# Kernel optimization log

Measured on AMD Instinct MI355X. Metric: run time of the kernel, lower is better.

The kernel has to match this reference:

```python
import jax, jax.numpy as jnp
import numpy as np

TAU = 0.02
M = 5  # len(modality_types) + 1; modality 0 == padding


def setup_inputs() -> dict:
    B, Q, S, D = 64, 32, 256, 128
    key = jax.random.key(0)
    k0, k1, k2, k3, k4 = jax.random.split(key, 5)
    q = jax.random.normal(k0, (B, Q, D), dtype=jnp.float32)
    q = q / jnp.linalg.norm(q, axis=-1, keepdims=True)
    d = jax.random.normal(k1, (B, S, D), dtype=jnp.float32)
    d = d / jnp.linalg.norm(d, axis=-1, keepdims=True)
    # guarantee every modality 0..M-1 appears in each doc (first M tokens)
    head = jnp.tile(jnp.arange(M, dtype=jnp.int32), (B, 1))
    rest = jax.random.randint(k2, (B, S - M), 0, M, dtype=jnp.int32)
    modality_ids = jnp.concatenate([head, rest], axis=1)
    query_types = jax.random.randint(k3, (B,), 1, M, dtype=jnp.int32)  # in [1, M-1]
    lengths = jax.random.randint(k4, (B,), Q // 2, Q + 1)
    query_mask = jnp.arange(Q)[None, :] < lengths[:, None]
    return {"query_emb": q, "doc_emb": d, "modality_ids": modality_ids,
            "query_types": query_types, "query_mask": query_mask}


def _loss(query_emb, doc_emb, modality_ids, query_types, query_mask):
    B = query_emb.shape[0]
    idx = jnp.arange(B)
    # token-level similarity: (B, C, Q, S)
    base = jnp.einsum('bqd,csd->bcqs', query_emb, doc_emb)
    qnorm = jnp.maximum(query_mask.sum(axis=1), 1).astype(base.dtype)  # (B,)

    # agg (ColBERT max-sim): max over non-pad doc tokens, masked query sum
    nonpad = (modality_ids != 0)[None, :, None, :]
    agg_max = jnp.where(nonpad, base, -jnp.inf).max(axis=-1)           # (B, C, Q)
    sim = (agg_max * query_mask[:, None, :].astype(base.dtype)).sum(axis=-1)
    sim = sim / qnorm[:, None]                                          # (B, C)

    # _all_modality_sims: segmented max over s per modality, then sum over q
    per_mod = []
    for m in range(M):
        mask_m = (modality_ids == m)[None, :, None, :]
        per_mod.append(jnp.where(mask_m, base, -jnp.inf).max(axis=-1).sum(axis=-1))
    sims = jnp.stack(per_mod, axis=-1)                                  # (B, C, M)
    sims = sims / qnorm[:, None, None]

    # replace diagonal with the query's own modality score
    sim_fixed = sim.at[idx, idx].set(sims[idx, idx, query_types])

    # hard negatives: all (doc, modality) pairs except pad modality and own positive
    all_modal = sims.reshape(B, B * M)
    keep_mask = jnp.ones((B, B * M), dtype=bool)
    keep_mask = keep_mask.at[:, 0::M].set(False)
    keep_mask = keep_mask.at[idx, idx * M + query_types].set(False)
    n_keep = B * M - B - 1  # exact per-row count (query_types >= 1, no overlap)
    order = jnp.argsort((~keep_mask).astype(jnp.int32), axis=1, stable=True)[:, :n_keep]
    extras = jnp.take_along_axis(all_modal, order, axis=1)              # (B, n_keep)

    logits = jnp.concatenate([sim_fixed, extras], axis=1) / TAU
    # cross entropy with labels = arange(B) (positive is column b)
    return (jax.nn.logsumexp(logits, axis=1) - logits[idx, idx]).mean()


def reference(query_emb, doc_emb, modality_ids, query_types, query_mask):
    return _loss(query_emb, doc_emb, modality_ids, query_types, query_mask)
```

## Files before the change

kernel.cpp:

```cpp
#include <hip/hip_runtime.h>
#include <math.h>

#define TAU_F 0.02f
#define NB 64
#define NQ 32
#define NS 256
#define ND 128
#define MAXT 12
#define PERMSTRIDE 384

typedef __bf16 bf16x8 __attribute__((ext_vector_type(8)));
typedef float f32x16 __attribute__((ext_vector_type(16)));

#define OFF_TILEMOD 0u
#define OFF_TCOUNT  4096u
#define OFF_DFRAG   16384u
#define OFF_QFRAG   6307840u
#define OFF_SIMOUT  6832128u
#define OFF_RED     6914048u

__global__ __launch_bounds__(256) void
prep_frag_kernel(const float* __restrict__ qemb, const float* __restrict__ demb,
                 const int* __restrict__ mod,
                 __bf16* __restrict__ qfrag, __bf16* __restrict__ dfrag,
                 int* __restrict__ tilemod_g, int* __restrict__ tcount_g,
                 int* __restrict__ red) {
    int blk = blockIdx.x;
    int tid = threadIdx.x;
    int lane = tid & 63, wv = tid >> 6;
    int li32 = lane & 31, kh = lane >> 5;

    if (blk == 0 && tid == 0) { red[0] = 0; ((float*)red)[16] = 0.f; }

    if (blk >= NB) {
        int b = blk - NB;
#pragma unroll
        for (int i = 0; i < 2; ++i) {
            int kc = wv * 2 + i;
            int k0 = kc * 16 + kh * 8;
            const float* src = qemb + ((size_t)b * NQ + li32) * ND + k0;
            float4 a = *(const float4*)src;
            float4 bq = *(const float4*)(src + 4);
            bf16x8 o;
            o[0] = (__bf16)a.x;  o[1] = (__bf16)a.y;  o[2] = (__bf16)a.z;  o[3] = (__bf16)a.w;
            o[4] = (__bf16)bq.x; o[5] = (__bf16)bq.y; o[6] = (__bf16)bq.z; o[7] = (__bf16)bq.w;
            *(bf16x8*)(qfrag + (((size_t)b * 8 + kc) * 64 + lane) * 8) = o;
        }
        return;
    }

    int c = blk;
    __shared__ int smod[NS];
    __shared__ int sperm[PERMSTRIDE];
    __shared__ int counts[5], firsts[5], offs[5], padded[5];
    __shared__ int stilemod[MAXT];
    __shared__ int sT;

    if (tid < 5) { counts[tid] = 0; firsts[tid] = NS; }
    __syncthreads();
    int m_tok = mod[c * NS + tid];
    smod[tid] = m_tok;
    if (m_tok) { atomicAdd(&counts[m_tok], 1); atomicMin(&firsts[m_tok], tid); }
    __syncthreads();
    if (tid == 0) {
        int pos = 0;
        for (int m = 1; m <= 4; ++m) {
            offs[m] = pos;
            int p = (counts[m] + 31) & ~31;
            padded[m] = p;
            for (int t = pos >> 5; t < (pos + p) >> 5; ++t) stilemod[t] = m;
            pos += p;
        }
        sT = pos >> 5;
        tcount_g[c] = pos >> 5;
    }
    __syncthreads();
    if (m_tok) {
        int rank = 0;
        for (int s = 0; s < tid; ++s) rank += (smod[s] == m_tok);
        sperm[offs[m_tok] + rank] = tid;
    }
    if (tid < 4) {
        int m = tid + 1;
        for (int p = counts[m]; p < padded[m]; ++p) sperm[offs[m] + p] = firsts[m];
    }
    __syncthreads();
    int T = sT;
    if (tid < T) tilemod_g[c * MAXT + tid] = stilemod[tid];

    for (int kc = wv; kc < 8; kc += 4) {
        int k0 = kc * 16 + kh * 8;
        for (int t = 0; t < T; ++t) {
            int srow = sperm[t * 32 + li32];
            const float* src = demb + ((size_t)c * NS + srow) * ND + k0;
            float4 a = *(const float4*)src;
            float4 bq = *(const float4*)(src + 4);
            bf16x8 o;
            o[0] = (__bf16)a.x;  o[1] = (__bf16)a.y;  o[2] = (__bf16)a.z;  o[3] = (__bf16)a.w;
            o[4] = (__bf16)bq.x; o[5] = (__bf16)bq.y; o[6] = (__bf16)bq.z; o[7] = (__bf16)bq.w;
            *(bf16x8*)(dfrag + (((size_t)(c * MAXT + t) * 8 + kc) * 64 + lane) * 8) = o;
        }
    }
}

__global__ __launch_bounds__(256) void
main_kernel(const __bf16* __restrict__ dfrag, const __bf16* __restrict__ qfrag,
            const int* __restrict__ tilemod, const int* __restrict__ tcount,
            const int* __restrict__ qmask, float* __restrict__ simout) {
    int blk = blockIdx.x;
    int c  = (blk & 7) * 8 + (blk >> 8);
    int bp = (blk >> 3) & 31;
    int b0 = bp * 2;
    int tid = threadIdx.x;
    int lane = tid & 63, wv = tid >> 6;

    bf16x8 bfrag[2][8];
#pragma unroll
    for (int bi = 0; bi < 2; ++bi)
#pragma unroll
        for (int kc = 0; kc < 8; ++kc)
            bfrag[bi][kc] = *(const bf16x8*)(qfrag + (((size_t)(b0 + bi) * 8 + kc) * 64 + lane) * 8);

    float vmax[2][4];
#pragma unroll
    for (int bi = 0; bi < 2; ++bi)
#pragma unroll
        for (int m = 0; m < 4; ++m) vmax[bi][m] = -1e30f;

    int T = tcount[c];
    for (int t = wv; t < T; t += 4) {
        bf16x8 af[8];
#pragma unroll
        for (int kc = 0; kc < 8; ++kc)
            af[kc] = *(const bf16x8*)(dfrag + (((size_t)(c * MAXT + t) * 8 + kc) * 64 + lane) * 8);
        int tm = tilemod[c * MAXT + t];
#pragma unroll
        for (int bi = 0; bi < 2; ++bi) {
            f32x16 acc = {0.f,0.f,0.f,0.f,0.f,0.f,0.f,0.f,0.f,0.f,0.f,0.f,0.f,0.f,0.f,0.f};
#pragma unroll
            for (int kc = 0; kc < 8; ++kc)
                acc = __builtin_amdgcn_mfma_f32_32x32x16_bf16(af[kc], bfrag[bi][kc], acc, 0, 0, 0);
            float v = acc[0];
#pragma unroll
            for (int r = 1; r < 16; ++r) v = fmaxf(v, acc[r]);
            v = fmaxf(v, __shfl_xor(v, 32, 64));
            switch (tm) {
            case 1:  vmax[bi][0] = fmaxf(vmax[bi][0], v); break;
            case 2:  vmax[bi][1] = fmaxf(vmax[bi][1], v); break;
            case 3:  vmax[bi][2] = fmaxf(vmax[bi][2], v); break;
            default: vmax[bi][3] = fmaxf(vmax[bi][3], v); break;
            }
        }
    }

    __shared__ float lv[4][2][4][32];
    if (lane < 32) {
#pragma unroll
        for (int bi = 0; bi < 2; ++bi)
#pragma unroll
            for (int m = 0; m < 4; ++m) lv[wv][bi][m][lane] = vmax[bi][m];
    }
    __syncthreads();
    __shared__ float l2s[2][4][32];
    {
        int bi = tid >> 7, m = (tid >> 5) & 3, q = tid & 31;
        float v = fmaxf(fmaxf(lv[0][bi][m][q], lv[1][bi][m][q]),
                        fmaxf(lv[2][bi][m][q], lv[3][bi][m][q]));
        l2s[bi][m][q] = v;
    }
    __syncthreads();
    if (tid < 64) {
        int bi = tid >> 5, q = tid & 31;
        float m1 = l2s[bi][0][q], m2 = l2s[bi][1][q];
        float m3 = l2s[bi][2][q], m4 = l2s[bi][3][q];
        int b = b0 + bi;
        float agg = fmaxf(fmaxf(m1, m2), fmaxf(m3, m4));
        float s0 = (qmask[b * NQ + q] != 0) ? agg : 0.f;
        float s1 = m1, s2 = m2, s3 = m3, s4 = m4;
#pragma unroll
        for (int off = 16; off >= 1; off >>= 1) {
            s0 += __shfl_xor(s0, off, 64);
            s1 += __shfl_xor(s1, off, 64);
            s2 += __shfl_xor(s2, off, 64);
            s3 += __shfl_xor(s3, off, 64);
            s4 += __shfl_xor(s4, off, 64);
        }
        if (q == 0) {
            float* o = simout + ((size_t)b * NB + c) * 5;
            o[0] = s0; o[1] = s1; o[2] = s2; o[3] = s3; o[4] = s4;
        }
    }
}

__global__ __launch_bounds__(256) void
loss_kernel(const float* __restrict__ simout, const int* __restrict__ qtypes,
            const int* __restrict__ qmask, int* __restrict__ red,
            float* __restrict__ out) {
    int r = blockIdx.x;
    int tid = threadIdx.x;
    int lane = tid & 63, wv = tid >> 6;

    __shared__ float sv[320];
    for (int i = tid; i < 320; i += 256) sv[i] = simout[(size_t)r * 320 + i];

    __shared__ int scnt;
    if (wv == 0) {
        int on = (lane < NQ) ? (qmask[r * NQ + lane] != 0) : 0;
        unsigned long long bal = __ballot(on);
        if (lane == 0) scnt = __popcll(bal);
    }
    __syncthreads();
    int cq = scnt;
    float scale = 1.0f / (TAU_F * (float)(cq > 0 ? cq : 1));
    int skip = r * 5;

    __shared__ float wred[4];
    float mx = -1e30f;
    for (int i = tid; i < 320; i += 256)
        if (i != skip) mx = fmaxf(mx, sv[i] * scale);
#pragma unroll
    for (int off = 32; off >= 1; off >>= 1) mx = fmaxf(mx, __shfl_xor(mx, off, 64));
    if (lane == 0) wred[wv] = mx;
    __syncthreads();
    mx = fmaxf(fmaxf(wred[0], wred[1]), fmaxf(wred[2], wred[3]));

    float sum = 0.f;
    for (int i = tid; i < 320; i += 256)
        if (i != skip) sum += expf(sv[i] * scale - mx);
#pragma unroll
    for (int off = 32; off >= 1; off >>= 1) sum += __shfl_xor(sum, off, 64);
    __syncthreads();
    if (lane == 0) wred[wv] = sum;
    __syncthreads();

    if (tid == 0) {
        float tot = wred[0] + wred[1] + wred[2] + wred[3];
        float pos = sv[r * 5 + qtypes[r]] * scale;
        float lr = (logf(tot) + mx - pos) * (1.0f / NB);
        float* acc = (float*)red + 16;
        float ret = atomicAdd(acc, lr);
        int bump = 1 + (ret > 1e37f ? 1 : 0);
        int old = atomicAdd(red, bump);
        if (old == NB - 1) {
            float v = atomicAdd(acc, 0.f);
            out[0] = v;
        }
    }
}

extern "C" void kernel_launch(void* const* d_in, const int* in_sizes, int n_in,
                              void* d_out, int out_size, void* d_ws, size_t ws_size,
                              hipStream_t stream) {
    const float* qemb   = (const float*)d_in[0];
    const float* demb   = (const float*)d_in[1];
    const int*   mod    = (const int*)d_in[2];
    const int*   qtypes = (const int*)d_in[3];
    const int*   qmask  = (const int*)d_in[4];

    char* ws = (char*)d_ws;
    int*    tilemod = (int*)(ws + OFF_TILEMOD);
    int*    tcount  = (int*)(ws + OFF_TCOUNT);
    __bf16* dfrag   = (__bf16*)(ws + OFF_DFRAG);
    __bf16* qfrag   = (__bf16*)(ws + OFF_QFRAG);
    float*  simout  = (float*)(ws + OFF_SIMOUT);
    int*    red     = (int*)(ws + OFF_RED);

    prep_frag_kernel<<<2 * NB, 256, 0, stream>>>(qemb, demb, mod, qfrag, dfrag,
                                                 tilemod, tcount, red);
    main_kernel<<<2048, 256, 0, stream>>>(dfrag, qfrag, tilemod, tcount, qmask, simout);
    loss_kernel<<<NB, 256, 0, stream>>>(simout, qtypes, qmask, red, (float*)d_out);
}
```

Measured before the change: 94.91 us.

## Fuse loss computation into main kernel via last-block-done counters per query pair

Removes the separate loss kernel launch. Each main-kernel block bumps a per-query-pair counter, and the last of the 64 blocks for that pair reads the pair's similarity rows with atomic loads and computes both cross-entropy terms. A global counter then picks the final block, which writes the mean. This saves one launch and its dependency gap, at the cost of extra atomics and a serialized tail in the last blocks, plus a reliance on memory ordering between blocks.

Result: slower. 101.1 us (+6.5%).

```diff
diff --git a/kernel.cpp b/kernel.cpp
--- a/kernel.cpp
+++ b/kernel.cpp
@@ -30,7 +30,11 @@
     int lane = tid & 63, wv = tid >> 6;
     int li32 = lane & 31, kh = lane >> 5;
 
-    if (blk == 0 && tid == 0) { red[0] = 0; ((float*)red)[16] = 0.f; }
+    if (blk == 0 && tid < 34) {
+        if (tid < 32) red[tid] = 0;
+        else if (tid == 32) red[32] = 0;
+        else ((float*)red)[48] = 0.f;
+    }
 
     if (blk >= NB) {
         int b = blk - NB;
@@ -106,7 +110,9 @@
 __global__ __launch_bounds__(256) void
 main_kernel(const __bf16* __restrict__ dfrag, const __bf16* __restrict__ qfrag,
             const int* __restrict__ tilemod, const int* __restrict__ tcount,
-            const int* __restrict__ qmask, float* __restrict__ simout) {
+            const int* __restrict__ qmask, const int* __restrict__ qtypes,
+            float* __restrict__ simout, int* __restrict__ red,
+            float* __restrict__ out) {
     int blk = blockIdx.x;
     int c  = (blk & 7) * 8 + (blk >> 8);
     int bp = (blk >> 3) & 31;
@@ -187,62 +193,70 @@
         }
         if (q == 0) {
             float* o = simout + ((size_t)b * NB + c) * 5;
-            o[0] = s0; o[1] = s1; o[2] = s2; o[3] = s3; o[4] = s4;
-        }
-    }
-}
-
-__global__ __launch_bounds__(256) void
-loss_kernel(const float* __restrict__ simout, const int* __restrict__ qtypes,
-            const int* __restrict__ qmask, int* __restrict__ red,
-            float* __restrict__ out) {
-    int r = blockIdx.x;
-    int tid = threadIdx.x;
-    int lane = tid & 63, wv = tid >> 6;
+            __hip_atomic_store(&o[0], s0, __ATOMIC_RELAXED, __HIP_MEMORY_SCOPE_AGENT);
+            __hip_atomic_store(&o[1], s1, __ATOMIC_RELAXED, __HIP_MEMORY_SCOPE_AGENT);
+            __hip_atomic_store(&o[2], s2, __ATOMIC_RELAXED, __HIP_MEMORY_SCOPE_AGENT);
+            __hip_atomic_store(&o[3], s3, __ATOMIC_RELAXED, __HIP_MEMORY_SCOPE_AGENT);
+            __hip_atomic_store(&o[4], s4, __ATOMIC_RELAXED, __HIP_MEMORY_SCOPE_AGENT);
+        }
+    }
+
+    __shared__ int swin;
+    __syncthreads();
+    if (tid == 0) swin = (atomicAdd(&red[bp], 1) == 63);
+    __syncthreads();
+    if (!swin) return;
 
     __shared__ float sv[320];
-    for (int i = tid; i < 320; i += 256) sv[i] = simout[(size_t)r * 320 + i];
-
+    __shared__ float wred[4];
     __shared__ int scnt;
-    if (wv == 0) {
-        int on = (lane < NQ) ? (qmask[r * NQ + lane] != 0) : 0;
-        unsigned long long bal = __ballot(on);
-        if (lane == 0) scnt = __popcll(bal);
-    }
-    __syncthreads();
-    int cq = scnt;
-    float scale = 1.0f / (TAU_F * (float)(cq > 0 ? cq : 1));
-    int skip = r * 5;
-
-    __shared__ float wred[4];
-    float mx = -1e30f;
-    for (int i = tid; i < 320; i += 256)
-        if (i != skip) mx = fmaxf(mx, sv[i] * scale);
-#pragma unroll
-    for (int off = 32; off >= 1; off >>= 1) mx = fmaxf(mx, __shfl_xor(mx, off, 64));
-    if (lane == 0) wred[wv] = mx;
-    __syncthreads();
-    mx = fmaxf(fmaxf(wred[0], wred[1]), fmaxf(wred[2], wred[3]));
-
-    float sum = 0.f;
-    for (int i = tid; i < 320; i += 256)
-        if (i != skip) sum += expf(sv[i] * scale - mx);
-#pragma unroll
-    for (int off = 32; off >= 1; off >>= 1) sum += __shfl_xor(sum, off, 64);
-    __syncthreads();
-    if (lane == 0) wred[wv] = sum;
-    __syncthreads();
-
+    float lr_sum = 0.f;
+#pragma unroll
+    for (int bi = 0; bi < 2; ++bi) {
+        int r = b0 + bi;
+        for (int i = tid; i < 320; i += 256)
+            sv[i] = __hip_atomic_load(&simout[(size_t)r * 320 + i],
+                                      __ATOMIC_RELAXED, __HIP_MEMORY_SCOPE_AGENT);
+        if (wv == 0) {
+            int on = (lane < NQ) ? (qmask[r * NQ + lane] != 0) : 0;
+            unsigned long long bal = __ballot(on);
+            if (lane == 0) scnt = __popcll(bal);
+        }
+        __syncthreads();
+        int cq = scnt;
+        float scale = 1.0f / (TAU_F * (float)(cq > 0 ? cq : 1));
+        int skip = r * 5;
+        float mx = -1e30f;
+        for (int i = tid; i < 320; i += 256)
+            if (i != skip) mx = fmaxf(mx, sv[i] * scale);
+#pragma unroll
+        for (int off = 32; off >= 1; off >>= 1) mx = fmaxf(mx, __shfl_xor(mx, off, 64));
+        if (lane == 0) wred[wv] = mx;
+        __syncthreads();
+        mx = fmaxf(fmaxf(wred[0], wred[1]), fmaxf(wred[2], wred[3]));
+        float sum = 0.f;
+        for (int i = tid; i < 320; i += 256)
+            if (i != skip) sum += expf(sv[i] * scale - mx);
+#pragma unroll
+        for (int off = 32; off >= 1; off >>= 1) sum += __shfl_xor(sum, off, 64);
+        __syncthreads();
+        if (lane == 0) wred[wv] = sum;
+        __syncthreads();
+        if (tid == 0) {
+            float tot = wred[0] + wred[1] + wred[2] + wred[3];
+            float pos = sv[r * 5 + qtypes[r]] * scale;
+            lr_sum += (logf(tot) + mx - pos) * (1.0f / NB);
+        }
+        __syncthreads();
+    }
     if (tid == 0) {
-        float tot = wred[0] + wred[1] + wred[2] + wred[3];
-        float pos = sv[r * 5 + qtypes[r]] * scale;
-        float lr = (logf(tot) + mx - pos) * (1.0f / NB);
-        float* acc = (float*)red + 16;
-        float ret = atomicAdd(acc, lr);
+        float* gacc = (float*)red + 48;
+        float ret = atomicAdd(gacc, lr_sum);
+        asm volatile("s_waitcnt vmcnt(0)" ::: "memory");
         int bump = 1 + (ret > 1e37f ? 1 : 0);
-        int old = atomicAdd(red, bump);
-        if (old == NB - 1) {
-            float v = atomicAdd(acc, 0.f);
+        int old = atomicAdd(&red[32], bump);
+        if (old == 31) {
+            float v = atomicAdd(gacc, 0.f);
             out[0] = v;
         }
     }
@@ -267,6 +281,6 @@
 
     prep_frag_kernel<<<2 * NB, 256, 0, stream>>>(qemb, demb, mod, qfrag, dfrag,
                                                  tilemod, tcount, red);
-    main_kernel<<<2048, 256, 0, stream>>>(dfrag, qfrag, tilemod, tcount, qmask, simout);
-    loss_kernel<<<NB, 256, 0, stream>>>(simout, qtypes, qmask, red, (float*)d_out);
+    main_kernel<<<2048, 256, 0, stream>>>(dfrag, qfrag, tilemod, tcount, qmask,
+                                          qtypes, simout, red, (float*)d_out);
 }
```

## Share doc tiles across waves via double-buffered LDS, split queries per wave

Applied to the files above, without the earlier changes.

Each block of the main kernel now handles one document and eight queries, with each wave owning two queries. The block streams the doc's 32-token tiles through a double-buffered shared-memory buffer, prefetching the next tile into registers while the current one is multiplied. This replaces per-wave global loads of a disjoint subset of tiles and the cross-wave shared-memory max reduction. The grid shrinks from 2048 to 512 blocks, so there is less parallelism, and each tile step now has a block-wide barrier, in exchange for four times the reuse of each doc tile.

New measurement: 90.65 us. -4.5%, faster.

```diff
diff --git a/kernel.cpp b/kernel.cpp
--- a/kernel.cpp
+++ b/kernel.cpp
@@ -103,16 +103,18 @@
     }
 }
 
-__global__ __launch_bounds__(256) void
+__global__ __launch_bounds__(256, 2) void
 main_kernel(const __bf16* __restrict__ dfrag, const __bf16* __restrict__ qfrag,
             const int* __restrict__ tilemod, const int* __restrict__ tcount,
             const int* __restrict__ qmask, float* __restrict__ simout) {
     int blk = blockIdx.x;
-    int c  = (blk & 7) * 8 + (blk >> 8);
-    int bp = (blk >> 3) & 31;
-    int b0 = bp * 2;
+    int xcd = blk & 7;
+    int idx = blk >> 3;
+    int c   = xcd * 8 + (idx & 7);
+    int bq  = idx >> 3;
     int tid = threadIdx.x;
     int lane = tid & 63, wv = tid >> 6;
+    int b0 = bq * 8 + wv * 2;
 
     bf16x8 bfrag[2][8];
 #pragma unroll
@@ -121,59 +123,68 @@
         for (int kc = 0; kc < 8; ++kc)
             bfrag[bi][kc] = *(const bf16x8*)(qfrag + (((size_t)(b0 + bi) * 8 + kc) * 64 + lane) * 8);
 
+    __shared__ __bf16 sbuf[2][8 * 64 * 8];
+
+    int T = tcount[c];
+    const __bf16* dbase = dfrag + (size_t)c * MAXT * 4096;
+
+    {
+        const __bf16* src = dbase;
+        *(bf16x8*)&sbuf[0][(size_t)tid * 8]          = *(const bf16x8*)(src + (size_t)tid * 8);
+        *(bf16x8*)&sbuf[0][2048 + (size_t)tid * 8]   = *(const bf16x8*)(src + 2048 + (size_t)tid * 8);
+    }
+    __syncthreads();
+
     float vmax[2][4];
 #pragma unroll
     for (int bi = 0; bi < 2; ++bi)
 #pragma unroll
         for (int m = 0; m < 4; ++m) vmax[bi][m] = -1e30f;
 
-    int T = tcount[c];
-    for (int t = wv; t < T; t += 4) {
-        bf16x8 af[8];
-#pragma unroll
-        for (int kc = 0; kc < 8; ++kc)
-            af[kc] = *(const bf16x8*)(dfrag + (((size_t)(c * MAXT + t) * 8 + kc) * 64 + lane) * 8);
+    int cur = 0;
+    for (int t = 0; t < T; ++t) {
+        bf16x8 p0, p1;
+        bool pf = (t + 1 < T);
+        if (pf) {
+            const __bf16* src = dbase + (size_t)(t + 1) * 4096;
+            p0 = *(const bf16x8*)(src + (size_t)tid * 8);
+            p1 = *(const bf16x8*)(src + 2048 + (size_t)tid * 8);
+        }
+
         int tm = tilemod[c * MAXT + t];
-#pragma unroll
-        for (int bi = 0; bi < 2; ++bi) {
-            f32x16 acc = {0.f,0.f,0.f,0.f,0.f,0.f,0.f,0.f,0.f,0.f,0.f,0.f,0.f,0.f,0.f,0.f};
-#pragma unroll
-            for (int kc = 0; kc < 8; ++kc)
-                acc = __builtin_amdgcn_mfma_f32_32x32x16_bf16(af[kc], bfrag[bi][kc], acc, 0, 0, 0);
-            float v = acc[0];
-#pragma unroll
-            for (int r = 1; r < 16; ++r) v = fmaxf(v, acc[r]);
-            v = fmaxf(v, __shfl_xor(v, 32, 64));
-            switch (tm) {
-            case 1:  vmax[bi][0] = fmaxf(vmax[bi][0], v); break;
-            case 2:  vmax[bi][1] = fmaxf(vmax[bi][1], v); break;
-            case 3:  vmax[bi][2] = fmaxf(vmax[bi][2], v); break;
-            default: vmax[bi][3] = fmaxf(vmax[bi][3], v); break;
-            }
-        }
-    }
-
-    __shared__ float lv[4][2][4][32];
-    if (lane < 32) {
-#pragma unroll
-        for (int bi = 0; bi < 2; ++bi)
-#pragma unroll
-            for (int m = 0; m < 4; ++m) lv[wv][bi][m][lane] = vmax[bi][m];
-    }
-    __syncthreads();
-    __shared__ float l2s[2][4][32];
-    {
-        int bi = tid >> 7, m = (tid >> 5) & 3, q = tid & 31;
-        float v = fmaxf(fmaxf(lv[0][bi][m][q], lv[1][bi][m][q]),
-                        fmaxf(lv[2][bi][m][q], lv[3][bi][m][q]));
-        l2s[bi][m][q] = v;
-    }
-    __syncthreads();
-    if (tid < 64) {
-        int bi = tid >> 5, q = tid & 31;
-        float m1 = l2s[bi][0][q], m2 = l2s[bi][1][q];
-        float m3 = l2s[bi][2][q], m4 = l2s[bi][3][q];
+        f32x16 acc0 = {0.f,0.f,0.f,0.f,0.f,0.f,0.f,0.f,0.f,0.f,0.f,0.f,0.f,0.f,0.f,0.f};
+        f32x16 acc1 = acc0;
+#pragma unroll
+        for (int kc = 0; kc < 8; ++kc) {
+            bf16x8 af = *(const bf16x8*)&sbuf[cur][(kc * 64 + lane) * 8];
+            acc0 = __builtin_amdgcn_mfma_f32_32x32x16_bf16(af, bfrag[0][kc], acc0, 0, 0, 0);
+            acc1 = __builtin_amdgcn_mfma_f32_32x32x16_bf16(af, bfrag[1][kc], acc1, 0, 0, 0);
+        }
+        float v0 = acc0[0], v1 = acc1[0];
+#pragma unroll
+        for (int r = 1; r < 16; ++r) { v0 = fmaxf(v0, acc0[r]); v1 = fmaxf(v1, acc1[r]); }
+        v0 = fmaxf(v0, __shfl_xor(v0, 32, 64));
+        v1 = fmaxf(v1, __shfl_xor(v1, 32, 64));
+        switch (tm) {
+        case 1:  vmax[0][0] = fmaxf(vmax[0][0], v0); vmax[1][0] = fmaxf(vmax[1][0], v1); break;
+        case 2:  vmax[0][1] = fmaxf(vmax[0][1], v0); vmax[1][1] = fmaxf(vmax[1][1], v1); break;
+        case 3:  vmax[0][2] = fmaxf(vmax[0][2], v0); vmax[1][2] = fmaxf(vmax[1][2], v1); break;
+        default: vmax[0][3] = fmaxf(vmax[0][3], v0); vmax[1][3] = fmaxf(vmax[1][3], v1); break;
+        }
+
+        if (pf) {
+            *(bf16x8*)&sbuf[cur ^ 1][(size_t)tid * 8]        = p0;
+            *(bf16x8*)&sbuf[cur ^ 1][2048 + (size_t)tid * 8] = p1;
+        }
+        __syncthreads();
+        cur ^= 1;
+    }
+
+    int q = lane & 31;
+#pragma unroll
+    for (int bi = 0; bi < 2; ++bi) {
         int b = b0 + bi;
+        float m1 = vmax[bi][0], m2 = vmax[bi][1], m3 = vmax[bi][2], m4 = vmax[bi][3];
         float agg = fmaxf(fmaxf(m1, m2), fmaxf(m3, m4));
         float s0 = (qmask[b * NQ + q] != 0) ? agg : 0.f;
         float s1 = m1, s2 = m2, s3 = m3, s4 = m4;
@@ -185,7 +196,7 @@
             s3 += __shfl_xor(s3, off, 64);
             s4 += __shfl_xor(s4, off, 64);
         }
-        if (q == 0) {
+        if (lane == 0) {
             float* o = simout + ((size_t)b * NB + c) * 5;
             o[0] = s0; o[1] = s1; o[2] = s2; o[3] = s3; o[4] = s4;
         }
@@ -267,6 +278,6 @@
 
     prep_frag_kernel<<<2 * NB, 256, 0, stream>>>(qemb, demb, mod, qfrag, dfrag,
                                                  tilemod, tcount, red);
-    main_kernel<<<2048, 256, 0, stream>>>(dfrag, qfrag, tilemod, tcount, qmask, simout);
+    main_kernel<<<512, 256, 0, stream>>>(dfrag, qfrag, tilemod, tcount, qmask, simout);
     loss_kernel<<<NB, 256, 0, stream>>>(simout, qtypes, qmask, red, (float*)d_out);
 }
```
